# Optimization experiments

Measured on AMD Instinct MI355X. Metric: run time of the kernel, lower is better.

The kernel has to match this reference:

```python
import jax, jax.numpy as jnp
import numpy as np
from jax import lax

B, S, D, H = 256, 1024, 64, 128


def setup_inputs() -> dict:
    key = jax.random.key(0)
    ks = jax.random.split(key, 11)
    s_in = 1.0 / np.sqrt(H)  # torch RNNCell/Linear init scale (uniform bound); normal scale ok for testing
    return {
        "inputs": jax.random.normal(ks[0], (B, S, D), jnp.float32),
        "Wih_fw": jax.random.normal(ks[1], (H, D), jnp.float32) * s_in,
        "Whh_fw": jax.random.normal(ks[2], (H, H), jnp.float32) * s_in,
        "bih_fw": jax.random.normal(ks[3], (H,), jnp.float32) * s_in,
        "bhh_fw": jax.random.normal(ks[4], (H,), jnp.float32) * s_in,
        "Wih_bw": jax.random.normal(ks[5], (H, D), jnp.float32) * s_in,
        "Whh_bw": jax.random.normal(ks[6], (H, H), jnp.float32) * s_in,
        "bih_bw": jax.random.normal(ks[7], (H,), jnp.float32) * s_in,
        "bhh_bw": jax.random.normal(ks[8], (H,), jnp.float32) * s_in,
        "fc_W": jax.random.normal(ks[9], (1, 2 * H), jnp.float32) * (1.0 / np.sqrt(2 * H)),
        "fc_b": jnp.zeros((1,), jnp.float32),
    }


def _run_dir(inputs, Wih, Whh, bih, bhh, reverse):
    # Precompute input projection for all timesteps: [B,S,H]
    xp = jnp.einsum('bsd,hd->bsh', inputs, Wih) + bih + bhh
    WhhT = Whh.T

    def step(h, x_t):  # x_t: [B,H]
        h_new = jnp.tanh(x_t + h @ WhhT)
        return h_new, h_new

    h0 = jnp.zeros((inputs.shape[0], Whh.shape[0]), inputs.dtype)
    # scan over time; reverse=True processes t = S-1..0 and emits outputs in
    # original time order, matching torch's output_bw[::-1] stacking.
    _, ys = lax.scan(step, h0, jnp.swapaxes(xp, 0, 1), reverse=reverse)
    return jnp.swapaxes(ys, 0, 1)  # [B,S,H]


def reference(inputs, Wih_fw, Whh_fw, bih_fw, bhh_fw,
              Wih_bw, Whh_bw, bih_bw, bhh_bw, fc_W, fc_b):
    out_fw = _run_dir(inputs, Wih_fw, Whh_fw, bih_fw, bhh_fw, reverse=False)
    out_bw = _run_dir(inputs, Wih_bw, Whh_bw, bih_bw, bhh_bw, reverse=True)
    outputs = jnp.concatenate([out_fw, out_bw], axis=2)  # [B,S,2H]
    outputs = outputs @ fc_W.T + fc_b  # [B,S,1]
    return jnp.squeeze(outputs, -1)  # [B,S]
```

## Files before the change

### kernel.cpp

```cpp
#include <hip/hip_runtime.h>

namespace {

constexpr int kS = 1024;
constexpr int kD = 64;
constexpr int kH = 128;

typedef __attribute__((ext_vector_type(2))) _Float16 half2v;
typedef __attribute__((ext_vector_type(4))) float f32x4;
typedef __attribute__((ext_vector_type(8))) _Float16 half8;

__device__ __forceinline__ float fdot2(unsigned w, unsigned h, float acc) {
#if __has_builtin(__builtin_amdgcn_fdot2)
  return __builtin_amdgcn_fdot2(__builtin_bit_cast(half2v, w),
                                __builtin_bit_cast(half2v, h), acc, false);
#else
  float d;
  asm("v_dot2_f32_f16 %0, %1, %2, %3" : "=v"(d) : "v"(w), "v"(h), "v"(acc));
  return d;
#endif
}

__device__ __forceinline__ unsigned pk16(float a, float b) {
  half2v h;
  h.x = (_Float16)a;
  h.y = (_Float16)b;
  return __builtin_bit_cast(unsigned, h);
}

__device__ __forceinline__ float fast_tanh(float x) {
  x = fminf(fmaxf(x, -15.f), 15.f);
  float e = __expf(2.f * x);
  return (e - 1.f) * __builtin_amdgcn_rcpf(e + 1.f);
}

#if __has_builtin(__builtin_amdgcn_mov_dpp)
__device__ __forceinline__ float lane_xor1(float v) {
  return __int_as_float(__builtin_amdgcn_mov_dpp(__float_as_int(v), 0xB1, 0xF, 0xF, true));
}
#else
__device__ __forceinline__ float lane_xor1(float v) {
  return __int_as_float(__builtin_amdgcn_ds_swizzle(__float_as_int(v), 0x041F));
}
#endif

__device__ __forceinline__ void stage_chunk(const char* g, unsigned* lds, int L) {
#pragma unroll
  for (int k = 0; k < 8; ++k) {
    __builtin_amdgcn_global_load_lds(
        (const __attribute__((address_space(1))) void*)(g + k * 1024 + L * 16),
        (__attribute__((address_space(3))) void*)(lds + k * 256), 16, 0, 0);
  }
}


__global__ __launch_bounds__(256, 2) void xproj_kernel(
    const float* __restrict__ inputs,
    const float* __restrict__ Wih_fw, const float* __restrict__ bih_fw,
    const float* __restrict__ bhh_fw,
    const float* __restrict__ Wih_bw, const float* __restrict__ bih_bw,
    const float* __restrict__ bhh_bw,
    _Float16* __restrict__ xp) {
  __shared__ _Float16 Wl[256 * 80];
  __shared__ _Float16 xl[128 * 80];
  __shared__ float biasl[256];

  const int tid = threadIdx.x;
  const int b = blockIdx.x;
  const int w = tid >> 6;
  const int lane = tid & 63;
  const int n16 = lane & 15;
  const int q = lane >> 4;

  {
    const int jd = tid;
    const float* src = (jd < kH) ? (Wih_fw + jd * kD) : (Wih_bw + (jd - kH) * kD);
    const float4* s4 = (const float4*)src;
#pragma unroll
    for (int k = 0; k < 8; ++k) {
      float4 a = s4[2 * k], c = s4[2 * k + 1];
      half8 h;
      h[0] = (_Float16)a.x; h[1] = (_Float16)a.y; h[2] = (_Float16)a.z; h[3] = (_Float16)a.w;
      h[4] = (_Float16)c.x; h[5] = (_Float16)c.y; h[6] = (_Float16)c.z; h[7] = (_Float16)c.w;
      *(half8*)&Wl[jd * 80 + k * 8] = h;
    }
    biasl[jd] = (jd < kH) ? (bih_fw[jd] + bhh_fw[jd])
                          : (bih_bw[jd - kH] + bhh_bw[jd - kH]);
  }

  for (int ch = 0; ch < 8; ++ch) {
    __syncthreads();
    {
      const int tl = tid >> 1, hf = tid & 1;
      const float4* s4 = (const float4*)(inputs +
          ((size_t)b * kS + ch * 128 + tl) * kD + hf * 32);
#pragma unroll
      for (int k = 0; k < 4; ++k) {
        float4 a = s4[2 * k], c = s4[2 * k + 1];
        half8 h;
        h[0] = (_Float16)a.x; h[1] = (_Float16)a.y; h[2] = (_Float16)a.z; h[3] = (_Float16)a.w;
        h[4] = (_Float16)c.x; h[5] = (_Float16)c.y; h[6] = (_Float16)c.z; h[7] = (_Float16)c.w;
        *(half8*)&xl[tl * 80 + hf * 32 + k * 8] = h;
      }
    }
    __syncthreads();

    half8 bf0[4], bf1[4];
    float bs[4];
#pragma unroll
    for (int nn = 0; nn < 4; ++nn) {
      const int jd = (w * 4 + nn) * 16 + n16;
      bf0[nn] = *(const half8*)&Wl[jd * 80 + q * 8];
      bf1[nn] = *(const half8*)&Wl[jd * 80 + q * 8 + 32];
      bs[nn] = biasl[jd];
    }

#pragma unroll 2
    for (int m = 0; m < 8; ++m) {
      const int trow = m * 16 + n16;
      const half8 a0 = *(const half8*)&xl[trow * 80 + q * 8];
      const half8 a1 = *(const half8*)&xl[trow * 80 + q * 8 + 32];
#pragma unroll
      for (int nn = 0; nn < 4; ++nn) {
        f32x4 acc = {0.f, 0.f, 0.f, 0.f};
        acc = __builtin_amdgcn_mfma_f32_16x16x32_f16(a0, bf0[nn], acc, 0, 0, 0);
        acc = __builtin_amdgcn_mfma_f32_16x16x32_f16(a1, bf1[nn], acc, 0, 0, 0);
        const int jd = (w * 4 + nn) * 16 + n16;
        const int dir = jd >> 7, j = jd & 127;
        const size_t slab = (size_t)(dir * 256 + b) * (kS * kH);
#pragma unroll
        for (int r = 0; r < 4; ++r) {
          const int t = ch * 128 + m * 16 + q * 4 + r;
          const int tt = dir ? (kS - 1 - t) : t;
          xp[slab + (size_t)(tt >> 5) * (32 * kH) + (tt & 31) * kH + j] =
              (_Float16)(acc[r] + bs[nn]);
        }
      }
    }
  }
}

__global__ __launch_bounds__(64, 1) void birnn_step_kernel(
    const _Float16* __restrict__ xp,
    const float* __restrict__ Whh_fw, const float* __restrict__ Whh_bw,
    const float* __restrict__ fcW, const float* __restrict__ fcb,
    float* __restrict__ out) {
  const int dir = blockIdx.x >> 8;
  const int b = blockIdx.x & 255;
  const int L = threadIdx.x;

  __shared__ unsigned jrn[32 * 68];
  __shared__ unsigned xbuf[2][2048];
  __shared__ unsigned fcwl[64];
  __shared__ float outbuf[kS];

  const float* __restrict__ Whh = dir ? Whh_bw : Whh_fw;

  unsigned w0[64], w1[64];
  {
    const float* r0 = Whh + (size_t)(2 * L) * kH;
    const float* r1 = Whh + (size_t)(2 * L + 1) * kH;
#pragma unroll
    for (int k = 0; k < 64; ++k) {
      w0[k] = pk16(r0[2 * k], r0[2 * k + 1]);
      w1[k] = pk16(r1[2 * k], r1[2 * k + 1]);
    }
  }
  fcwl[L] = pk16(fcW[dir * kH + 2 * L], fcW[dir * kH + 2 * L + 1]);
  jrn[31 * 68 + L] = 0;

  const char* slab = (const char*)(xp + (size_t)(dir * 256 + b) * (kS * kH));
  stage_chunk(slab, &xbuf[0][0], L);
  stage_chunk(slab + 8192, &xbuf[1][0], L);
  asm volatile("s_waitcnt vmcnt(0)" ::: "memory");

  for (int c = 0; c < 32; ++c) {
    const unsigned* xb = &xbuf[c & 1][0];

#pragma unroll 2
    for (int s = 0; s < 32; ++s) {
      const int prev = (s + 31) & 31;
      const uint4* hr = (const uint4*)&jrn[prev * 68];
      float a0 = 0.f, a1 = 0.f, a2 = 0.f, a3 = 0.f;
      float c0 = 0.f, c1 = 0.f, c2 = 0.f, c3 = 0.f;
#pragma unroll
      for (int g = 0; g < 16; ++g) {
        const uint4 hv = hr[g];
        a0 = fdot2(w0[4 * g + 0], hv.x, a0);
        c0 = fdot2(w1[4 * g + 0], hv.x, c0);
        a1 = fdot2(w0[4 * g + 1], hv.y, a1);
        c1 = fdot2(w1[4 * g + 1], hv.y, c1);
        a2 = fdot2(w0[4 * g + 2], hv.z, a2);
        c2 = fdot2(w1[4 * g + 2], hv.z, c2);
        a3 = fdot2(w0[4 * g + 3], hv.w, a3);
        c3 = fdot2(w1[4 * g + 3], hv.w, c3);
      }
      const half2v xh = __builtin_bit_cast(half2v, xb[s * 64 + L]);
      const float va = ((a0 + a1) + (a2 + a3)) + (float)xh.x;
      const float vb = ((c0 + c1) + (c2 + c3)) + (float)xh.y;
      jrn[s * 68 + L] = pk16(fast_tanh(va), fast_tanh(vb));
    }

    {
      const int tl = L >> 1, jh = L & 1;
      const uint4* rp = (const uint4*)&jrn[tl * 68 + jh * 32];
      const uint4* fp = (const uint4*)&fcwl[jh * 32];
      float acc = 0.f;
#pragma unroll
      for (int k = 0; k < 8; ++k) {
        const uint4 hv = rp[k];
        const uint4 fw = fp[k];
        acc = fdot2(fw.x, hv.x, acc);
        acc = fdot2(fw.y, hv.y, acc);
        acc = fdot2(fw.z, hv.z, acc);
        acc = fdot2(fw.w, hv.w, acc);
      }
      acc += lane_xor1(acc);
      if (jh == 0) outbuf[c * 32 + tl] = acc;
    }

    if (c < 30) {
      stage_chunk(slab + (size_t)(c + 2) * 8192, &xbuf[c & 1][0], L);
      asm volatile("s_waitcnt vmcnt(8)" ::: "memory");
    } else if (c == 30) {
      asm volatile("s_waitcnt vmcnt(0)" ::: "memory");
    }
  }

  const float fcb0 = (dir == 0) ? fcb[0] : 0.f;
#pragma unroll
  for (int k = 0; k < 16; ++k) {
    const int t = L + 64 * k;
    const int td = dir ? (kS - 1 - t) : t;
    atomicAdd(&out[(size_t)b * kS + td], outbuf[t] + fcb0);
  }
}

}

extern "C" void kernel_launch(void* const* d_in, const int* in_sizes, int n_in,
                              void* d_out, int out_size, void* d_ws, size_t ws_size,
                              hipStream_t stream) {
  (void)in_sizes; (void)n_in; (void)ws_size;
  const float* inputs = (const float*)d_in[0];
  const float* Wih_fw = (const float*)d_in[1];
  const float* Whh_fw = (const float*)d_in[2];
  const float* bih_fw = (const float*)d_in[3];
  const float* bhh_fw = (const float*)d_in[4];
  const float* Wih_bw = (const float*)d_in[5];
  const float* Whh_bw = (const float*)d_in[6];
  const float* bih_bw = (const float*)d_in[7];
  const float* bhh_bw = (const float*)d_in[8];
  const float* fc_W   = (const float*)d_in[9];
  const float* fc_b   = (const float*)d_in[10];
  float* out = (float*)d_out;
  _Float16* xpw = (_Float16*)d_ws;

  hipMemsetAsync(out, 0, (size_t)out_size * sizeof(float), stream);

  hipLaunchKernelGGL(xproj_kernel, dim3(256), dim3(256), 0, stream,
                     inputs, Wih_fw, bih_fw, bhh_fw, Wih_bw, bih_bw, bhh_bw, xpw);
  hipLaunchKernelGGL(birnn_step_kernel, dim3(512), dim3(64), 0, stream,
                     xpw, Whh_fw, Whh_bw, fc_W, fc_b, out);
}
```

Before: 567.6 us.

## Process two batch rows per RNN block to interleave independent recurrences

Each step-kernel block now runs the recurrence for two batch elements at once, reusing the register-resident Whh weights across both. Their dot-product chains are interleaved to expose more instruction-level parallelism and hide LDS and ALU latency. The grid is halved to 256 single-wave blocks, so each CU likely holds one wave instead of two. That may leave SIMDs idle and lengthen the serial path per step. LDS use per block doubles.

New measurement: 1.170 ms. +106.2%, slower.

```diff
diff --git a/kernel.cpp b/kernel.cpp
--- a/kernel.cpp
+++ b/kernel.cpp
@@ -145,14 +145,15 @@
     const float* __restrict__ Whh_fw, const float* __restrict__ Whh_bw,
     const float* __restrict__ fcW, const float* __restrict__ fcb,
     float* __restrict__ out) {
-  const int dir = blockIdx.x >> 8;
-  const int b = blockIdx.x & 255;
+  const int dir = blockIdx.x >> 7;
+  const int bp = blockIdx.x & 127;
+  const int b0 = 2 * bp, b1 = 2 * bp + 1;
   const int L = threadIdx.x;
 
-  __shared__ unsigned jrn[32 * 68];
-  __shared__ unsigned xbuf[2][2048];
+  __shared__ unsigned jrn[2][32 * 68];
+  __shared__ unsigned xbuf[2][2][2048];
   __shared__ unsigned fcwl[64];
-  __shared__ float outbuf[kS];
+  __shared__ float outbuf[2][kS];
 
   const float* __restrict__ Whh = dir ? Whh_bw : Whh_fw;
 
@@ -167,61 +168,90 @@
     }
   }
   fcwl[L] = pk16(fcW[dir * kH + 2 * L], fcW[dir * kH + 2 * L + 1]);
-  jrn[31 * 68 + L] = 0;
-
-  const char* slab = (const char*)(xp + (size_t)(dir * 256 + b) * (kS * kH));
-  stage_chunk(slab, &xbuf[0][0], L);
-  stage_chunk(slab + 8192, &xbuf[1][0], L);
-  asm volatile("s_waitcnt vmcnt(0)" ::: "memory");
+  jrn[0][31 * 68 + L] = 0;
+  jrn[1][31 * 68 + L] = 0;
+
+  const char* slabA = (const char*)(xp + (size_t)(dir * 256 + b0) * (kS * kH));
+  const char* slabB = (const char*)(xp + (size_t)(dir * 256 + b1) * (kS * kH));
+  stage_chunk(slabA, &xbuf[0][0][0], L);
+  stage_chunk(slabB, &xbuf[1][0][0], L);
+  stage_chunk(slabA + 8192, &xbuf[0][1][0], L);
+  stage_chunk(slabB + 8192, &xbuf[1][1][0], L);
+  asm volatile("s_waitcnt vmcnt(16)" ::: "memory");
 
   for (int c = 0; c < 32; ++c) {
-    const unsigned* xb = &xbuf[c & 1][0];
+    const unsigned* xbA = &xbuf[0][c & 1][0];
+    const unsigned* xbB = &xbuf[1][c & 1][0];
 
 #pragma unroll 2
     for (int s = 0; s < 32; ++s) {
       const int prev = (s + 31) & 31;
-      const uint4* hr = (const uint4*)&jrn[prev * 68];
-      float a0 = 0.f, a1 = 0.f, a2 = 0.f, a3 = 0.f;
-      float c0 = 0.f, c1 = 0.f, c2 = 0.f, c3 = 0.f;
+      const uint4* hrA = (const uint4*)&jrn[0][prev * 68];
+      const uint4* hrB = (const uint4*)&jrn[1][prev * 68];
+      float aA0 = 0.f, aA1 = 0.f, aA2 = 0.f, aA3 = 0.f;
+      float cA0 = 0.f, cA1 = 0.f, cA2 = 0.f, cA3 = 0.f;
+      float aB0 = 0.f, aB1 = 0.f, aB2 = 0.f, aB3 = 0.f;
+      float cB0 = 0.f, cB1 = 0.f, cB2 = 0.f, cB3 = 0.f;
 #pragma unroll
       for (int g = 0; g < 16; ++g) {
-        const uint4 hv = hr[g];
-        a0 = fdot2(w0[4 * g + 0], hv.x, a0);
-        c0 = fdot2(w1[4 * g + 0], hv.x, c0);
-        a1 = fdot2(w0[4 * g + 1], hv.y, a1);
-        c1 = fdot2(w1[4 * g + 1], hv.y, c1);
-        a2 = fdot2(w0[4 * g + 2], hv.z, a2);
-        c2 = fdot2(w1[4 * g + 2], hv.z, c2);
-        a3 = fdot2(w0[4 * g + 3], hv.w, a3);
-        c3 = fdot2(w1[4 * g + 3], hv.w, c3);
-      }
-      const half2v xh = __builtin_bit_cast(half2v, xb[s * 64 + L]);
-      const float va = ((a0 + a1) + (a2 + a3)) + (float)xh.x;
-      const float vb = ((c0 + c1) + (c2 + c3)) + (float)xh.y;
-      jrn[s * 68 + L] = pk16(fast_tanh(va), fast_tanh(vb));
+        const uint4 hA = hrA[g];
+        const uint4 hB = hrB[g];
+        aA0 = fdot2(w0[4 * g + 0], hA.x, aA0);
+        aB0 = fdot2(w0[4 * g + 0], hB.x, aB0);
+        cA0 = fdot2(w1[4 * g + 0], hA.x, cA0);
+        cB0 = fdot2(w1[4 * g + 0], hB.x, cB0);
+        aA1 = fdot2(w0[4 * g + 1], hA.y, aA1);
+        aB1 = fdot2(w0[4 * g + 1], hB.y, aB1);
+        cA1 = fdot2(w1[4 * g + 1], hA.y, cA1);
+        cB1 = fdot2(w1[4 * g + 1], hB.y, cB1);
+        aA2 = fdot2(w0[4 * g + 2], hA.z, aA2);
+        aB2 = fdot2(w0[4 * g + 2], hB.z, aB2);
+        cA2 = fdot2(w1[4 * g + 2], hA.z, cA2);
+        cB2 = fdot2(w1[4 * g + 2], hB.z, cB2);
+        aA3 = fdot2(w0[4 * g + 3], hA.w, aA3);
+        aB3 = fdot2(w0[4 * g + 3], hB.w, aB3);
+        cA3 = fdot2(w1[4 * g + 3], hA.w, cA3);
+        cB3 = fdot2(w1[4 * g + 3], hB.w, cB3);
+      }
+      {
+        const half2v xhA = __builtin_bit_cast(half2v, xbA[s * 64 + L]);
+        const float va = ((aA0 + aA1) + (aA2 + aA3)) + (float)xhA.x;
+        const float vb = ((cA0 + cA1) + (cA2 + cA3)) + (float)xhA.y;
+        jrn[0][s * 68 + L] = pk16(fast_tanh(va), fast_tanh(vb));
+      }
+      {
+        const half2v xhB = __builtin_bit_cast(half2v, xbB[s * 64 + L]);
+        const float va = ((aB0 + aB1) + (aB2 + aB3)) + (float)xhB.x;
+        const float vb = ((cB0 + cB1) + (cB2 + cB3)) + (float)xhB.y;
+        jrn[1][s * 68 + L] = pk16(fast_tanh(va), fast_tanh(vb));
+      }
     }
 
     {
       const int tl = L >> 1, jh = L & 1;
-      const uint4* rp = (const uint4*)&jrn[tl * 68 + jh * 32];
       const uint4* fp = (const uint4*)&fcwl[jh * 32];
-      float acc = 0.f;
-#pragma unroll
-      for (int k = 0; k < 8; ++k) {
-        const uint4 hv = rp[k];
-        const uint4 fw = fp[k];
-        acc = fdot2(fw.x, hv.x, acc);
-        acc = fdot2(fw.y, hv.y, acc);
-        acc = fdot2(fw.z, hv.z, acc);
-        acc = fdot2(fw.w, hv.w, acc);
-      }
-      acc += lane_xor1(acc);
-      if (jh == 0) outbuf[c * 32 + tl] = acc;
+#pragma unroll
+      for (int ch2 = 0; ch2 < 2; ++ch2) {
+        const uint4* rp = (const uint4*)&jrn[ch2][tl * 68 + jh * 32];
+        float acc = 0.f;
+#pragma unroll
+        for (int k = 0; k < 8; ++k) {
+          const uint4 hv = rp[k];
+          const uint4 fw = fp[k];
+          acc = fdot2(fw.x, hv.x, acc);
+          acc = fdot2(fw.y, hv.y, acc);
+          acc = fdot2(fw.z, hv.z, acc);
+          acc = fdot2(fw.w, hv.w, acc);
+        }
+        acc += lane_xor1(acc);
+        if (jh == 0) outbuf[ch2][c * 32 + tl] = acc;
+      }
     }
 
     if (c < 30) {
-      stage_chunk(slab + (size_t)(c + 2) * 8192, &xbuf[c & 1][0], L);
-      asm volatile("s_waitcnt vmcnt(8)" ::: "memory");
+      stage_chunk(slabA + (size_t)(c + 2) * 8192, &xbuf[0][c & 1][0], L);
+      stage_chunk(slabB + (size_t)(c + 2) * 8192, &xbuf[1][c & 1][0], L);
+      asm volatile("s_waitcnt vmcnt(16)" ::: "memory");
     } else if (c == 30) {
       asm volatile("s_waitcnt vmcnt(0)" ::: "memory");
     }
@@ -232,7 +262,8 @@
   for (int k = 0; k < 16; ++k) {
     const int t = L + 64 * k;
     const int td = dir ? (kS - 1 - t) : t;
-    atomicAdd(&out[(size_t)b * kS + td], outbuf[t] + fcb0);
+    atomicAdd(&out[(size_t)b0 * kS + td], outbuf[0][t] + fcb0);
+    atomicAdd(&out[(size_t)b1 * kS + td], outbuf[1][t] + fcb0);
   }
 }
 
@@ -260,6 +291,6 @@
 
   hipLaunchKernelGGL(xproj_kernel, dim3(256), dim3(256), 0, stream,
                      inputs, Wih_fw, bih_fw, bhh_fw, Wih_bw, bih_bw, bhh_bw, xpw);
-  hipLaunchKernelGGL(birnn_step_kernel, dim3(512), dim3(64), 0, stream,
+  hipLaunchKernelGGL(birnn_step_kernel, dim3(256), dim3(64), 0, stream,
                      xpw, Whh_fw, Whh_bw, fc_W, fc_b, out);
 }
```
